# Performance work log

Hardware: AMD Instinct MI355X
Metric: run time of the kernel (lower is better)

## Reference

```python
import jax, jax.numpy as jnp
import numpy as np
from jax import lax

T, B, H, NF, FS = 512, 128, 512, 128, 5  # max_seq_len, batch, hidden, num_filters, filter_size


def setup_inputs() -> dict:
    key = jax.random.key(0)
    ks = jax.random.split(key, 16)
    inp = {
        "encoder_output": jax.random.normal(ks[0], (T, B, H), dtype=jnp.float32),
        "lengths": jax.random.randint(ks[1], (B,), 1, T + 1, dtype=jnp.int64 if jax.config.jax_enable_x64 else jnp.int32),
    }
    for w in range(1, FS + 1):
        inp[f"conv_w{w}"] = jax.random.normal(ks[1 + w], (NF, 1, H, w), dtype=jnp.float32) * 0.02
        inp[f"conv_b{w}"] = jnp.zeros((NF,), dtype=jnp.float32)
    inp["fc1_w"] = jax.random.normal(ks[12], (100, FS * NF), dtype=jnp.float32) * 0.05
    inp["fc1_b"] = jnp.zeros((100,), dtype=jnp.float32)
    inp["fc2_w"] = jax.random.normal(ks[13], (1, 100), dtype=jnp.float32) * 0.1
    inp["fc2_b"] = jnp.zeros((1,), dtype=jnp.float32)
    return inp


def _raw_reshape(x, L):
    # Faithful to torch .contiguous().view(1,1,H,-1) on a [L,H] slice:
    # row-major flatten of first L rows, reshaped to [H, L], zero-padded to [H, T].
    flat = x.reshape(-1)                       # [T*H]
    h = jnp.arange(H)[:, None]                 # [H,1]
    l = jnp.arange(T)[None, :]                 # [1,T]
    return jnp.where(l < L, flat[h * L + l], 0.0)  # [H,T]


def reference(encoder_output, lengths,
              conv_w1, conv_b1, conv_w2, conv_b2, conv_w3, conv_b3,
              conv_w4, conv_b4, conv_w5, conv_b5,
              fc1_w, fc1_b, fc2_w, fc2_b):
    # encoder_output: [T, B, H]; per-sample raw reshape to [H, T] (length-dependent)
    X = jax.vmap(_raw_reshape, in_axes=(1, 0))(encoder_output, lengths)  # [B,H,T]
    X4 = X[:, None, :, :]                                               # [B,1,H,T]
    Leff = jnp.maximum(lengths, FS)  # torch code zero-pads width to >= filter_size
    conv_ws = [conv_w1, conv_w2, conv_w3, conv_w4, conv_w5]
    conv_bs = [conv_b1, conv_b2, conv_b3, conv_b4, conv_b5]
    pools = []
    for w in range(1, FS + 1):
        out = lax.conv_general_dilated(
            X4, conv_ws[w - 1], window_strides=(1, 1), padding='VALID',
            dimension_numbers=('NCHW', 'OIHW', 'NCHW'))          # [B,NF,1,T-w+1]
        r = jax.nn.relu(out[:, :, 0, :] + conv_bs[w - 1][None, :, None])  # [B,NF,Tw]
        tpos = jnp.arange(T - w + 1)
        valid = tpos[None, :] < (Leff - w + 1)[:, None]          # [B,Tw]
        r = jnp.where(valid[:, None, :], r, 0.0)                 # relu>=0, so 0 is safe for max
        pools.append(r.max(axis=2))                              # [B,NF]
    feat = jnp.concatenate(pools, axis=1)                        # [B,FS*NF]
    fc1 = feat @ fc1_w.T + fc1_b
    fc2 = fc1 @ fc2_w.T + fc2_b
    probs = jax.nn.sigmoid(fc2)                                  # [B,1]
    return probs[:, None, :]                                     # [B,1,1] == torch.stack of [1,1]
```

## Files before the change

kernel.cpp:

```cpp
#include <hip/hip_runtime.h>
#include <hip/hip_bf16.h>

#define TT 512
#define BB 128
#define HH 512
#define NFC 128

typedef short v8s __attribute__((ext_vector_type(8)));
typedef float v4f __attribute__((ext_vector_type(4)));

__device__ __forceinline__ unsigned short f2bf(float x) {
    unsigned u = __float_as_uint(x);
    unsigned r = (u + 0x7fffu + ((u >> 16) & 1u)) >> 16;
    return (unsigned short)r;
}

__global__ void prep_all(const float* __restrict__ enc, const int* __restrict__ lengths,
                         unsigned short* __restrict__ Xg,
                         const float* __restrict__ w1, const float* __restrict__ w2,
                         const float* __restrict__ w3, const float* __restrict__ w4,
                         const float* __restrict__ w5, unsigned short* __restrict__ Wg,
                         float* __restrict__ pools,
                         const float* __restrict__ fc1w, const float* __restrict__ fc1b,
                         const float* __restrict__ fc2w, const float* __restrict__ fc2b,
                         float* __restrict__ v, int* __restrict__ wl) {
    int blk = blockIdx.x;
    int tid = threadIdx.x;
    if (blk < 8192) {
        __shared__ float tile[64 * 65];
        int b = blk >> 6;
        int lc = (blk >> 3) & 7;
        int hc = blk & 7;
        int L = lengths[b];
        int Leff = L > 5 ? L : 5;
        int l0 = lc * 64, h0 = hc * 64;
        if (l0 >= Leff + 127) return;
        int lx = tid & 63;
        int hq = tid >> 6;
        #pragma unroll
        for (int r = 0; r < 16; ++r) {
            int hl = hq * 16 + r;
            int l = l0 + lx;
            float val = 0.f;
            if (l < L) {
                int i = (h0 + hl) * L + l;
                val = enc[(i >> 9) * (BB * HH) + b * HH + (i & 511)];
            }
            tile[hl * 65 + lx] = val;
        }
        __syncthreads();
        int hg = tid & 15;
        #pragma unroll
        for (int r = 0; r < 4; ++r) {
            int lloc = (tid >> 4) + r * 16;
            int n = b * 512 + l0 + lloc;
            ushort4 pk;
            pk.x = f2bf(tile[(hg * 4 + 0) * 65 + lloc]);
            pk.y = f2bf(tile[(hg * 4 + 1) * 65 + lloc]);
            pk.z = f2bf(tile[(hg * 4 + 2) * 65 + lloc]);
            pk.w = f2bf(tile[(hg * 4 + 3) * 65 + lloc]);
            *(ushort4*)&Xg[n * 512 + h0 + hg * 4] = pk;
        }
    } else if (blk < 12288) {
        int idx = (blk - 8192) * 256 + tid;
        int s = idx >> 9, h = idx & 511;
        int f = s >> 4, sl = s & 15;
        float val = 0.f;
        if (sl < 15) {
            int w, j;
            if (sl < 1)       { w = 1; j = sl; }
            else if (sl < 3)  { w = 2; j = sl - 1; }
            else if (sl < 6)  { w = 3; j = sl - 3; }
            else if (sl < 10) { w = 4; j = sl - 6; }
            else              { w = 5; j = sl - 10; }
            const float* wp = (w == 1) ? w1 : (w == 2) ? w2 : (w == 3) ? w3 : (w == 4) ? w4 : w5;
            val = wp[f * (HH * w) + h * w + j];
        }
        Wg[idx] = f2bf(val);
    } else if (blk < 12608) {
        int i = (blk - 12288) * 256 + tid;
        if (i < BB * 5 * NFC) pools[i] = 0.f;
    } else if (blk == 12608) {
        for (int k = tid; k < 640; k += 256) {
            float s = 0.f;
            for (int o = 0; o < 100; ++o) s += fc2w[o] * fc1w[o * 640 + k];
            v[k] = s;
        }
        if (tid == 0) {
            float c = fc2b[0];
            for (int o = 0; o < 100; ++o) c += fc2w[o] * fc1b[o];
            v[640] = c;
        }
    } else {
        __shared__ int cnt;
        if (tid == 0) cnt = 0;
        __syncthreads();
        for (int it = tid; it < 640; it += 256) {
            int b = it / 5, tt = it % 5;
            int L = lengths[b];
            int Leff = L > 5 ? L : 5;
            int n0 = tt * 124 - ((tt >> 2) * 112);
            if (n0 < Leff) {
                int pos = atomicAdd(&cnt, 1);
                wl[pos] = (b << 3) | tt;
            }
        }
        __syncthreads();
        if (tid == 0) wl[640] = cnt;
    }
}

__global__ __launch_bounds__(256, 3)
void conv_gemm(const unsigned short* __restrict__ Wg, const unsigned short* __restrict__ Xg,
               const int* __restrict__ lengths, const int* __restrict__ wl,
               const float* __restrict__ cb1, const float* __restrict__ cb2,
               const float* __restrict__ cb3, const float* __restrict__ cb4,
               const float* __restrict__ cb5,
               float* __restrict__ pools) {
    __shared__ __align__(16) char smem[49152];
    unsigned short* ldsA = (unsigned short*)smem;
    unsigned short* ldsB = ldsA + 12288;
    float* Gs = (float*)smem;

    int cnt = wl[640];
    int wk = blockIdx.y;
    if (wk >= cnt) return;
    int item = wl[wk];
    int b = item >> 3, tt = item & 7;
    int mt = blockIdx.x;
    int n0 = tt * 124 - ((tt >> 2) * 112);
    int L = lengths[b];
    int Leff = L > 5 ? L : 5;

    int tid = threadIdx.x;
    int wid = tid >> 6, lane = tid & 63;
    int wm = wid >> 1, wn = wid & 1;
    int llo = lane & 15, quad = lane >> 4;
    int psw = quad ^ ((llo >> 1) & 3);

    int m0 = mt * 128;
    int nb0 = b * 512 + n0;

    v4f acc[4][4];
    #pragma unroll
    for (int i = 0; i < 4; ++i)
        #pragma unroll
        for (int j = 0; j < 4; ++j) acc[i][j] = v4f{0.f, 0.f, 0.f, 0.f};

    int srow = lane >> 2;
    int gchunk = (lane & 3) ^ ((lane >> 3) & 3);
    const unsigned short* gA = Wg + (m0 + wid * 32 + srow) * 512 + gchunk * 8;
    const unsigned short* gB = Xg + (nb0 + wid * 32 + srow) * 512 + gchunk * 8;
    int sdst = (wid * 32) * 32;

    #pragma unroll
    for (int p = 0; p < 2; ++p) {
        #pragma unroll
        for (int q = 0; q < 2; ++q) {
            __builtin_amdgcn_global_load_lds(
                (const __attribute__((address_space(1))) unsigned int*)(gA + q * (16 * 512) + p * 32),
                (__attribute__((address_space(3))) unsigned int*)&ldsA[p * 4096 + sdst + q * 512],
                16, 0, 0);
            __builtin_amdgcn_global_load_lds(
                (const __attribute__((address_space(1))) unsigned int*)(gB + q * (16 * 512) + p * 32),
                (__attribute__((address_space(3))) unsigned int*)&ldsB[p * 4096 + sdst + q * 512],
                16, 0, 0);
        }
    }

    int bcur = 0;
    #pragma unroll 1
    for (int kt = 0; kt < 16; ++kt) {
        if (kt < 14) {
            int bnx = bcur + 2; if (bnx >= 3) bnx -= 3;
            int ko = (kt + 2) * 32;
            #pragma unroll
            for (int q = 0; q < 2; ++q) {
                __builtin_amdgcn_global_load_lds(
                    (const __attribute__((address_space(1))) unsigned int*)(gA + q * (16 * 512) + ko),
                    (__attribute__((address_space(3))) unsigned int*)&ldsA[bnx * 4096 + sdst + q * 512],
                    16, 0, 0);
                __builtin_amdgcn_global_load_lds(
                    (const __attribute__((address_space(1))) unsigned int*)(gB + q * (16 * 512) + ko),
                    (__attribute__((address_space(3))) unsigned int*)&ldsB[bnx * 4096 + sdst + q * 512],
                    16, 0, 0);
            }
            asm volatile("s_waitcnt vmcnt(8)" ::: "memory");
        } else if (kt == 14) {
            asm volatile("s_waitcnt vmcnt(4)" ::: "memory");
        } else {
            asm volatile("s_waitcnt vmcnt(0)" ::: "memory");
        }
        __builtin_amdgcn_s_barrier();

        int boff = bcur * 4096;
        v8s Af[4], Bf[4];
        #pragma unroll
        for (int mi = 0; mi < 4; ++mi)
            Af[mi] = *(const v8s*)&ldsA[boff + (wm * 64 + mi * 16 + llo) * 32 + psw * 8];
        #pragma unroll
        for (int ni = 0; ni < 4; ++ni)
            Bf[ni] = *(const v8s*)&ldsB[boff + (wn * 64 + ni * 16 + llo) * 32 + psw * 8];
        asm volatile("s_waitcnt lgkmcnt(0)" ::: "memory");
        __builtin_amdgcn_sched_barrier(0);
        __builtin_amdgcn_s_barrier();

        __builtin_amdgcn_s_setprio(1);
        #pragma unroll
        for (int mi = 0; mi < 4; ++mi)
            #pragma unroll
            for (int ni = 0; ni < 4; ++ni)
                acc[mi][ni] = __builtin_amdgcn_mfma_f32_16x16x32_bf16(Af[mi], Bf[ni], acc[mi][ni], 0, 0, 0);
        __builtin_amdgcn_s_setprio(0);

        bcur += 1; if (bcur >= 3) bcur -= 3;
    }

    const int basew[6] = {0, 0, 1, 3, 6, 10};

    #pragma unroll
    for (int phase = 0; phase < 2; ++phase) {
        if (wm == phase) {
            #pragma unroll
            for (int mi = 0; mi < 4; ++mi)
                #pragma unroll
                for (int ni = 0; ni < 4; ++ni)
                    #pragma unroll
                    for (int r = 0; r < 4; ++r)
                        Gs[(mi * 16 + quad * 4 + r) * 129 + wn * 64 + ni * 16 + llo] = acc[mi][ni][r];
        }
        __syncthreads();
        {
            int fl = wid;
            int f = mt * 8 + phase * 4 + fl;
            #pragma unroll
            for (int w = 1; w <= 5; ++w) {
                float bias = (w == 1 ? cb1 : w == 2 ? cb2 : w == 3 ? cb3 : w == 4 ? cb4 : cb5)[f];
                int limv = Leff - w + 1 - n0;
                float vmax = -1.f;
                #pragma unroll
                for (int half = 0; half < 2; ++half) {
                    int t = half * 64 + lane;
                    if (t <= 128 - w && t < limv) {
                        float s = 0.f;
                        #pragma unroll
                        for (int j = 0; j < w; ++j)
                            s += Gs[(fl * 16 + basew[w] + j) * 129 + t + j];
                        s += bias;
                        s = fmaxf(s, 0.f);
                        vmax = fmaxf(vmax, s);
                    }
                }
                #pragma unroll
                for (int off = 32; off >= 1; off >>= 1)
                    vmax = fmaxf(vmax, __shfl_xor(vmax, off));
                if (lane == 0 && vmax >= 0.f)
                    atomicMax((int*)&pools[(b * 5 + (w - 1)) * NFC + f], __float_as_int(vmax));
            }
        }
        __syncthreads();
    }
}

__global__ void head(const float* __restrict__ pools, const float* __restrict__ v,
                     float* __restrict__ out) {
    int b = blockIdx.x;
    int tid = threadIdx.x;
    float s = 0.f;
    for (int k = tid; k < 640; k += 256) s += pools[b * 640 + k] * v[k];
    __shared__ float red[256];
    red[tid] = s;
    __syncthreads();
    for (int st = 128; st; st >>= 1) {
        if (tid < st) red[tid] += red[tid + st];
        __syncthreads();
    }
    if (tid == 0) out[b] = 1.f / (1.f + expf(-(red[0] + v[640])));
}

extern "C" void kernel_launch(void* const* d_in, const int* in_sizes, int n_in,
                              void* d_out, int out_size, void* d_ws, size_t ws_size,
                              hipStream_t stream) {
    const float* enc  = (const float*)d_in[0];
    const int* lens   = (const int*)d_in[1];
    const float* w1   = (const float*)d_in[2];
    const float* b1   = (const float*)d_in[3];
    const float* w2   = (const float*)d_in[4];
    const float* b2   = (const float*)d_in[5];
    const float* w3   = (const float*)d_in[6];
    const float* b3   = (const float*)d_in[7];
    const float* w4   = (const float*)d_in[8];
    const float* b4   = (const float*)d_in[9];
    const float* w5   = (const float*)d_in[10];
    const float* b5   = (const float*)d_in[11];
    const float* fc1w = (const float*)d_in[12];
    const float* fc1b = (const float*)d_in[13];
    const float* fc2w = (const float*)d_in[14];
    const float* fc2b = (const float*)d_in[15];
    float* out = (float*)d_out;

    unsigned short* Xg = (unsigned short*)d_ws;
    unsigned short* Wg = Xg + 33554432;
    float* pools  = (float*)(Wg + 1048576);
    float* vbuf   = pools + 81920;
    int* wlist    = (int*)(vbuf + 641);

    prep_all<<<12610, 256, 0, stream>>>(enc, lens, Xg, w1, w2, w3, w4, w5, Wg, pools,
                                        fc1w, fc1b, fc2w, fc2b, vbuf, wlist);
    conv_gemm<<<dim3(16, 640), 256, 0, stream>>>(Wg, Xg, lens, wlist, b1, b2, b3, b4, b5, pools);
    head<<<128, 256, 0, stream>>>(pools, vbuf, out);
}
```

Before: 381.4 us.

## Prepack conv weights in MFMA fragment order and load A directly to registers

The weight prep now writes the bf16 weight matrix in the exact per-wave MFMA fragment layout, so the GEMM kernel loads A fragments straight from global memory into registers with dwordx4 loads instead of staging them through LDS. Only the X (B operand) tiles remain in LDS, using a 4-deep ring, and one barrier per k-step is removed. LDS drops to about 33 KB and the launch bound is raised to 4 blocks per SU to improve occupancy. The risk is added global-load latency on the A path, plus the hand-written vmcnt counting, which must stay exact for correctness.

```diff
diff --git a/kernel.cpp b/kernel.cpp
--- a/kernel.cpp
+++ b/kernel.cpp
@@ -62,21 +62,28 @@
             *(ushort4*)&Xg[n * 512 + h0 + hg * 4] = pk;
         }
     } else if (blk < 12288) {
-        int idx = (blk - 8192) * 256 + tid;
-        int s = idx >> 9, h = idx & 511;
-        int f = s >> 4, sl = s & 15;
+        int o = (blk - 8192) * 256 + tid;
+        int j   = o & 7;
+        int ln  = (o >> 3) & 63;
+        int mi  = (o >> 9) & 3;
+        int kt  = (o >> 11) & 15;
+        int wmm = (o >> 15) & 1;
+        int mtt = o >> 16;
+        int row = mtt * 128 + wmm * 64 + mi * 16 + (ln & 15);
+        int k   = kt * 32 + (ln >> 4) * 8 + j;
+        int f = row >> 4, sl = row & 15;
         float val = 0.f;
         if (sl < 15) {
-            int w, j;
-            if (sl < 1)       { w = 1; j = sl; }
-            else if (sl < 3)  { w = 2; j = sl - 1; }
-            else if (sl < 6)  { w = 3; j = sl - 3; }
-            else if (sl < 10) { w = 4; j = sl - 6; }
-            else              { w = 5; j = sl - 10; }
+            int w, jj;
+            if (sl < 1)       { w = 1; jj = sl; }
+            else if (sl < 3)  { w = 2; jj = sl - 1; }
+            else if (sl < 6)  { w = 3; jj = sl - 3; }
+            else if (sl < 10) { w = 4; jj = sl - 6; }
+            else              { w = 5; jj = sl - 10; }
             const float* wp = (w == 1) ? w1 : (w == 2) ? w2 : (w == 3) ? w3 : (w == 4) ? w4 : w5;
-            val = wp[f * (HH * w) + h * w + j];
-        }
-        Wg[idx] = f2bf(val);
+            val = wp[f * (HH * w) + k * w + jj];
+        }
+        Wg[o] = f2bf(val);
     } else if (blk < 12608) {
         int i = (blk - 12288) * 256 + tid;
         if (i < BB * 5 * NFC) pools[i] = 0.f;
@@ -110,16 +117,15 @@
     }
 }
 
-__global__ __launch_bounds__(256, 3)
+__global__ __launch_bounds__(256, 4)
 void conv_gemm(const unsigned short* __restrict__ Wg, const unsigned short* __restrict__ Xg,
                const int* __restrict__ lengths, const int* __restrict__ wl,
                const float* __restrict__ cb1, const float* __restrict__ cb2,
                const float* __restrict__ cb3, const float* __restrict__ cb4,
                const float* __restrict__ cb5,
                float* __restrict__ pools) {
-    __shared__ __align__(16) char smem[49152];
-    unsigned short* ldsA = (unsigned short*)smem;
-    unsigned short* ldsB = ldsA + 12288;
+    __shared__ __align__(16) char smem[33024];
+    unsigned short* ldsB = (unsigned short*)smem;
     float* Gs = (float*)smem;
 
     int cnt = wl[640];
@@ -138,7 +144,6 @@
     int llo = lane & 15, quad = lane >> 4;
     int psw = quad ^ ((llo >> 1) & 3);
 
-    int m0 = mt * 128;
     int nb0 = b * 512 + n0;
 
     v4f acc[4][4];
@@ -149,18 +154,15 @@
 
     int srow = lane >> 2;
     int gchunk = (lane & 3) ^ ((lane >> 3) & 3);
-    const unsigned short* gA = Wg + (m0 + wid * 32 + srow) * 512 + gchunk * 8;
     const unsigned short* gB = Xg + (nb0 + wid * 32 + srow) * 512 + gchunk * 8;
     int sdst = (wid * 32) * 32;
 
+    const unsigned short* pA = Wg + (mt * 2 + wm) * 32768 + lane * 8;
+
     #pragma unroll
     for (int p = 0; p < 2; ++p) {
         #pragma unroll
         for (int q = 0; q < 2; ++q) {
-            __builtin_amdgcn_global_load_lds(
-                (const __attribute__((address_space(1))) unsigned int*)(gA + q * (16 * 512) + p * 32),
-                (__attribute__((address_space(3))) unsigned int*)&ldsA[p * 4096 + sdst + q * 512],
-                16, 0, 0);
             __builtin_amdgcn_global_load_lds(
                 (const __attribute__((address_space(1))) unsigned int*)(gB + q * (16 * 512) + p * 32),
                 (__attribute__((address_space(3))) unsigned int*)&ldsB[p * 4096 + sdst + q * 512],
@@ -168,53 +170,49 @@
         }
     }
 
-    int bcur = 0;
     #pragma unroll 1
     for (int kt = 0; kt < 16; ++kt) {
+        v8s Af0, Af1, Af2, Af3;
+        asm volatile("global_load_dwordx4 %0, %1, off"             : "=v"(Af0) : "v"(pA) : "memory");
+        asm volatile("global_load_dwordx4 %0, %1, off offset:1024" : "=v"(Af1) : "v"(pA) : "memory");
+        asm volatile("global_load_dwordx4 %0, %1, off offset:2048" : "=v"(Af2) : "v"(pA) : "memory");
+        asm volatile("global_load_dwordx4 %0, %1, off offset:3072" : "=v"(Af3) : "v"(pA) : "memory");
+        pA += 2048;
+
         if (kt < 14) {
-            int bnx = bcur + 2; if (bnx >= 3) bnx -= 3;
-            int ko = (kt + 2) * 32;
+            int bb = ((kt + 2) & 3) * 4096;
             #pragma unroll
-            for (int q = 0; q < 2; ++q) {
+            for (int q = 0; q < 2; ++q)
                 __builtin_amdgcn_global_load_lds(
-                    (const __attribute__((address_space(1))) unsigned int*)(gA + q * (16 * 512) + ko),
-                    (__attribute__((address_space(3))) unsigned int*)&ldsA[bnx * 4096 + sdst + q * 512],
+                    (const __attribute__((address_space(1))) unsigned int*)(gB + q * (16 * 512) + (kt + 2) * 32),
+                    (__attribute__((address_space(3))) unsigned int*)&ldsB[bb + sdst + q * 512],
                     16, 0, 0);
-                __builtin_amdgcn_global_load_lds(
-                    (const __attribute__((address_space(1))) unsigned int*)(gB + q * (16 * 512) + ko),
-                    (__attribute__((address_space(3))) unsigned int*)&ldsB[bnx * 4096 + sdst + q * 512],
-                    16, 0, 0);
-            }
-            asm volatile("s_waitcnt vmcnt(8)" ::: "memory");
-        } else if (kt == 14) {
-            asm volatile("s_waitcnt vmcnt(4)" ::: "memory");
-        } else {
-            asm volatile("s_waitcnt vmcnt(0)" ::: "memory");
-        }
+        }
+
+        asm volatile("s_waitcnt vmcnt(8)" ::: "memory");
         __builtin_amdgcn_s_barrier();
 
-        int boff = bcur * 4096;
-        v8s Af[4], Bf[4];
-        #pragma unroll
-        for (int mi = 0; mi < 4; ++mi)
-            Af[mi] = *(const v8s*)&ldsA[boff + (wm * 64 + mi * 16 + llo) * 32 + psw * 8];
+        int boff = (kt & 3) * 4096;
+        v8s Bf[4];
         #pragma unroll
         for (int ni = 0; ni < 4; ++ni)
             Bf[ni] = *(const v8s*)&ldsB[boff + (wn * 64 + ni * 16 + llo) * 32 + psw * 8];
-        asm volatile("s_waitcnt lgkmcnt(0)" ::: "memory");
+
+        if (kt < 14) asm volatile("s_waitcnt vmcnt(2)" ::: "memory");
+        else         asm volatile("s_waitcnt vmcnt(0)" ::: "memory");
         __builtin_amdgcn_sched_barrier(0);
-        __builtin_amdgcn_s_barrier();
 
         __builtin_amdgcn_s_setprio(1);
         #pragma unroll
-        for (int mi = 0; mi < 4; ++mi)
-            #pragma unroll
-            for (int ni = 0; ni < 4; ++ni)
-                acc[mi][ni] = __builtin_amdgcn_mfma_f32_16x16x32_bf16(Af[mi], Bf[ni], acc[mi][ni], 0, 0, 0);
+        for (int ni = 0; ni < 4; ++ni) {
+            acc[0][ni] = __builtin_amdgcn_mfma_f32_16x16x32_bf16(Af0, Bf[ni], acc[0][ni], 0, 0, 0);
+            acc[1][ni] = __builtin_amdgcn_mfma_f32_16x16x32_bf16(Af1, Bf[ni], acc[1][ni], 0, 0, 0);
+            acc[2][ni] = __builtin_amdgcn_mfma_f32_16x16x32_bf16(Af2, Bf[ni], acc[2][ni], 0, 0, 0);
+            acc[3][ni] = __builtin_amdgcn_mfma_f32_16x16x32_bf16(Af3, Bf[ni], acc[3][ni], 0, 0, 0);
+        }
         __builtin_amdgcn_s_setprio(0);
-
-        bcur += 1; if (bcur >= 3) bcur -= 3;
-    }
+    }
+    __syncthreads();
 
     const int basew[6] = {0, 0, 1, 3, 6, 10};
 
```

Result: faster. 359.6 us (-5.7%).
